# Kernel optimization log

Measured on AMD Instinct MI355X. Metric: run time of the kernel, lower is better.

## Reference

```python
import jax, jax.numpy as jnp
import numpy as np

N_HEADS = 16
KV_HEADS = 4
D_HEAD = 64
D_MODEL = 1024
NUM_BUCKETS = 32
MAX_DISTANCE = 128


def _relative_position_bucket(relative_position, num_buckets=NUM_BUCKETS, max_distance=MAX_DISTANCE):
    # Bidirectional (encoder) T5 bucket function.
    nb = num_buckets // 2
    rel_buckets = (relative_position > 0).astype(jnp.int32) * nb
    rp = jnp.abs(relative_position)
    max_exact = nb // 2
    is_small = rp < max_exact
    rp_safe = jnp.maximum(rp, 1).astype(jnp.float32)
    rp_large = max_exact + (
        jnp.log(rp_safe / max_exact) / np.log(max_distance / max_exact) * (nb - max_exact)
    ).astype(jnp.int32)
    rp_large = jnp.minimum(rp_large, nb - 1)
    return rel_buckets + jnp.where(is_small, rp, rp_large)


def compute_bias(rel_bias, q_len, k_len):
    context_pos = jnp.arange(q_len)[:, None]
    memory_pos = jnp.arange(k_len)[None, :]
    buckets = _relative_position_bucket(memory_pos - context_pos)  # [q, k]
    values = rel_bias[buckets]                                     # [q, k, H]
    return jnp.transpose(values, (2, 0, 1))[None]                  # [1, H, q, k]


def setup_inputs() -> dict:
    key = jax.random.key(0)
    ks = jax.random.split(key, 6)
    scale = D_MODEL ** -0.5
    return {
        "hidden_states": jax.random.normal(ks[0], (4, 2048, D_MODEL), jnp.float32),
        "Wq": jax.random.normal(ks[1], (N_HEADS * D_HEAD, D_MODEL), jnp.float32) * scale,
        "Wk": jax.random.normal(ks[2], (N_HEADS * D_HEAD, D_MODEL), jnp.float32) * scale,
        "Wv": jax.random.normal(ks[3], (N_HEADS * D_HEAD, D_MODEL), jnp.float32) * scale,
        "Wo": jax.random.normal(ks[4], (D_MODEL, N_HEADS * D_HEAD), jnp.float32) * scale,
        "rel_bias": jax.random.normal(ks[5], (NUM_BUCKETS, N_HEADS), jnp.float32),
    }


def reference(hidden_states, Wq, Wk, Wv, Wo, rel_bias):
    B, N, _ = hidden_states.shape
    G = N_HEADS // KV_HEADS
    # projections: torch Linear -> x @ W.T; shape to [b, heads, n, d]
    q = (hidden_states @ Wq.T).reshape(B, N, N_HEADS, D_HEAD).transpose(0, 2, 1, 3)
    k = (hidden_states @ Wk.T).reshape(B, N, N_HEADS, D_HEAD).transpose(0, 2, 1, 3)
    v = (hidden_states @ Wv.T).reshape(B, N, N_HEADS, D_HEAD).transpose(0, 2, 1, 3)
    # split heads into (g, h) groups with h = kv_heads as inner index
    gq = q.reshape(B, G, KV_HEADS, N, D_HEAD)
    gk = k.reshape(B, G, KV_HEADS, N, D_HEAD).mean(axis=1)  # [b, h, n, d]
    gv = v.reshape(B, G, KV_HEADS, N, D_HEAD).mean(axis=1)
    # NOTE: einsum sums queries over the group axis g (faithful to source)
    scores = jnp.einsum('bghnd,bhsd->bhns', gq, gk)
    bias = compute_bias(rel_bias, N, N)                      # [1, H, n, n]
    gbias = bias.reshape(1, G, KV_HEADS, N, N).mean(axis=1)  # [1, h, n, n]
    scores = scores + gbias
    attn = jax.nn.softmax(scores.astype(jnp.float32), axis=-1).astype(scores.dtype)
    out = jnp.einsum('bhns,bhsd->bhnd', attn, gv)
    out = out.transpose(0, 2, 1, 3).reshape(B, N, KV_HEADS * D_HEAD)
    out = jnp.tile(out, (1, 1, G))  # repeat 'b s d -> b s (g d)'
    return out @ Wo.T
```

## Files before the change

kernel.cpp:

```cpp
#include <hip/hip_runtime.h>
#include <math.h>

typedef _Float16 half_t;
typedef _Float16 half4 __attribute__((ext_vector_type(4)));
typedef _Float16 half8 __attribute__((ext_vector_type(8)));
typedef float f32x4 __attribute__((ext_vector_type(4)));

#define LOG2E 1.44269504088896f

__device__ __forceinline__ void gload16(const void* g, void* l) {
    __builtin_amdgcn_global_load_lds(
        (const __attribute__((address_space(1))) unsigned int*)g,
        (__attribute__((address_space(3))) unsigned int*)l, 16, 0, 0);
}

__global__ __launch_bounds__(256) void prep(const float* __restrict__ hs,
                     const float* __restrict__ Wq, const float* __restrict__ Wk,
                     const float* __restrict__ Wv, const float* __restrict__ Wo,
                     const float* __restrict__ rb,
                     half_t* __restrict__ hsh,
                     half_t* __restrict__ Wqkv, half_t* __restrict__ Wo_e,
                     float* __restrict__ btab) {
    if (blockIdx.x < 4096) {
        int i = (blockIdx.x * 256 + threadIdx.x) * 8;
        f32x4 a = *(const f32x4*)&hs[i];
        f32x4 b = *(const f32x4*)&hs[i + 4];
        half8 o;
        #pragma unroll
        for (int j = 0; j < 4; ++j) { o[j] = (half_t)a[j]; o[4 + j] = (half_t)b[j]; }
        *(half8*)&hsh[i] = o;
        return;
    }
    int idx = (blockIdx.x - 4096) * 256 + threadIdx.x;
    if (idx < 768 * 1024) {
        int row = idx >> 10, col = idx & 1023;
        int sec = row >> 8;
        int r = row & 255;
        int h = r >> 6, d = r & 63;
        const float* W = (sec == 0) ? Wq : ((sec == 1) ? Wk : Wv);
        float s = 0.f;
        #pragma unroll
        for (int g = 0; g < 4; ++g) s += W[((g * 4 + h) * 64 + d) * 1024 + col];
        s *= (sec == 0) ? LOG2E : 0.25f;
        Wqkv[idx] = (half_t)s;
    }
    if (idx < 1024 * 256) {
        int m = idx >> 8, c = idx & 255;
        float s = 0.f;
        #pragma unroll
        for (int g = 0; g < 4; ++g) s += Wo[m * 1024 + g * 256 + c];
        Wo_e[idx] = (half_t)s;
    }
    if (idx < 4 * 4096) {
        int h = idx >> 12, dpos = idx & 4095;
        int delta = dpos - 2048;
        int bucket = (delta > 0) ? 16 : 0;
        int ad = delta < 0 ? -delta : delta;
        if (ad < 8) bucket += ad;
        else {
            int large = 8 + (int)(logf((float)ad * 0.125f) / logf(16.0f) * 8.0f);
            bucket += (large < 15) ? large : 15;
        }
        float s = 0.f;
        #pragma unroll
        for (int g = 0; g < 4; ++g) s += rb[bucket * 16 + g * 4 + h];
        btab[idx] = s * 0.25f * LOG2E;
    }
}

__global__ __launch_bounds__(256) void gemm_nt_mfma(const half_t* __restrict__ A,
                                                    const half_t* __restrict__ B,
                                                    void* __restrict__ Cptr,
                                                    int M, int N, int K, int store_half,
                                                    half_t* __restrict__ vtp) {
    __shared__ __attribute__((aligned(16))) half_t As[128 * 64];
    __shared__ __attribute__((aligned(16))) half_t Bs[64 * 64];
    int tid = threadIdx.x;
    int w = tid >> 6, lane = tid & 63;
    int c = lane & 15, quad = lane >> 4;
    int rowBase = blockIdx.y * 128, colBase = blockIdx.x * 64;
    int wr = (w & 1) * 64, wc = (w >> 1) * 32;

    f32x4 acc[4][2];
    #pragma unroll
    for (int i = 0; i < 4; ++i)
        #pragma unroll
        for (int j = 0; j < 2; ++j) acc[i][j] = (f32x4)(0.f);

    int srow = tid >> 3;
    int kcs = ((tid & 7) ^ (srow & 7)) * 8;
    int rx = c & 7;

    for (int k0 = 0; k0 < K; k0 += 64) {
        __syncthreads();
        #pragma unroll
        for (int p = 0; p < 4; ++p)
            gload16(&A[(size_t)(rowBase + srow + 32 * p) * K + k0 + kcs],
                    &As[p * 2048 + w * 512]);
        #pragma unroll
        for (int p = 0; p < 2; ++p)
            gload16(&B[(size_t)(colBase + srow + 32 * p) * K + k0 + kcs],
                    &Bs[p * 2048 + w * 512]);
        __syncthreads();

        #pragma unroll
        for (int kh = 0; kh < 2; ++kh) {
            int xk = ((quad + 4 * kh) ^ rx) * 8;
            half8 af[4], bf[2];
            #pragma unroll
            for (int i = 0; i < 4; ++i)
                af[i] = *(const half8*)&As[(wr + i * 16 + c) * 64 + xk];
            #pragma unroll
            for (int j = 0; j < 2; ++j)
                bf[j] = *(const half8*)&Bs[(wc + j * 16 + c) * 64 + xk];
            #pragma unroll
            for (int i = 0; i < 4; ++i)
                #pragma unroll
                for (int j = 0; j < 2; ++j)
                    acc[i][j] = __builtin_amdgcn_mfma_f32_16x16x32_f16(af[i], bf[j], acc[i][j], 0, 0, 0);
        }
    }

    if (vtp && colBase >= 512) {
        int h = (colBase - 512) >> 6;
        #pragma unroll
        for (int i = 0; i < 4; ++i)
            #pragma unroll
            for (int j = 0; j < 2; ++j) {
                int row0 = rowBase + wr + i * 16 + quad * 4;
                int dd = wc + j * 16 + c;
                int b = row0 >> 11, n = row0 & 2047;
                half4 pk;
                #pragma unroll
                for (int reg = 0; reg < 4; ++reg) pk[reg] = (half_t)acc[i][j][reg];
                *(half4*)&vtp[((size_t)((b * 4 + h) * 64 + dd)) * 2048 + n] = pk;
            }
        return;
    }

    #pragma unroll
    for (int i = 0; i < 4; ++i)
        #pragma unroll
        for (int j = 0; j < 2; ++j)
            #pragma unroll
            for (int reg = 0; reg < 4; ++reg) {
                size_t row = rowBase + wr + i * 16 + quad * 4 + reg;
                size_t col = colBase + wc + j * 16 + c;
                if (store_half) ((half_t*)Cptr)[row * N + col] = (half_t)acc[i][j][reg];
                else            ((float*)Cptr)[row * N + col] = acc[i][j][reg];
            }
}

__global__ __launch_bounds__(256) void attn(const half_t* __restrict__ qkv,
                                            const half_t* __restrict__ vt,
                                            const float* __restrict__ btab,
                                            half_t* __restrict__ Opart,
                                            float* __restrict__ ml) {
    __shared__ __attribute__((aligned(16))) half_t Ks[64 * 64];
    __shared__ __attribute__((aligned(16))) half_t Vts[64 * 64];
    __shared__ __attribute__((aligned(16))) half_t Ps[4 * 16 * 72];
    __shared__ float bstat[1152];

    int tid = threadIdx.x;
    int w = tid >> 6, lane = tid & 63;
    int c = lane & 15, quad = lane >> 4;
    int qt = blockIdx.x, h = blockIdx.y;
    int b = blockIdx.z >> 1, s = blockIdx.z & 1;
    int q0 = qt * 64;
    int bh = b * 4 + h;
    int k0g = s * 1024;

    const half_t* qrow = qkv + (size_t)(b * 2048 + q0 + w * 16 + c) * 768 + h * 64;
    half8 qf0 = *(const half8*)(qrow + quad * 8);
    half8 qf1 = *(const half8*)(qrow + 32 + quad * 8);

    float cpos = btab[h * 4096 + 4095];
    float cneg = btab[h * 4096];

    int bbase = k0g - q0 - 63 + 2048;
    for (int j = tid; j < 1152; j += 256) {
        int gi = bbase + j;
        gi = gi < 0 ? 0 : (gi > 4095 ? 4095 : gi);
        bstat[j] = btab[h * 4096 + gi];
    }

    int srow = tid >> 3;
    int kcs = ((tid & 7) ^ (srow & 7)) * 8;
    const half_t* gK = qkv + (size_t)(b * 2048 + k0g + srow) * 768 + 256 + h * 64 + kcs;
    const half_t* gV = vt + (size_t)(bh * 64 + srow) * 2048 + k0g + kcs;

    f32x4 O[4];
    #pragma unroll
    for (int i = 0; i < 4; ++i) O[i] = (f32x4)(0.f);
    float mrow = -1e30f, lrow = 0.f;

    int rx = c & 7;
    half_t* pw = &Ps[w * 16 * 72];

    for (int it = 0; it < 16; ++it) {
        int ktg = k0g + it * 64;
        __syncthreads();
        {
            const half_t* gKt = gK + (size_t)(it * 64) * 768;
            const half_t* gVt = gV + it * 64;
            gload16(gKt,                     &Ks[w * 512]);
            gload16(gKt + (size_t)32 * 768,  &Ks[2048 + w * 512]);
            gload16(gVt,                     &Vts[w * 512]);
            gload16(gVt + 32 * 2048,         &Vts[2048 + w * 512]);
        }
        __syncthreads();

        f32x4 ST[4];
        #pragma unroll
        for (int kb = 0; kb < 4; ++kb) {
            int row = kb * 16 + c;
            half8 kf0 = *(const half8*)&Ks[row * 64 + (quad ^ rx) * 8];
            half8 kf1 = *(const half8*)&Ks[row * 64 + ((quad + 4) ^ rx) * 8];
            f32x4 a = (f32x4)(0.f);
            a = __builtin_amdgcn_mfma_f32_16x16x32_f16(kf0, qf0, a, 0, 0, 0);
            a = __builtin_amdgcn_mfma_f32_16x16x32_f16(kf1, qf1, a, 0, 0, 0);
            ST[kb] = a;
        }

        float cb;
        if (ktg >= q0 + 191) {
            cb = cpos;
        } else if (ktg + 191 <= q0) {
            cb = cneg;
        } else {
            cb = 0.f;
            int jb = it * 64 + 63 - (w * 16 + c);
            #pragma unroll
            for (int kb = 0; kb < 4; ++kb)
                #pragma unroll
                for (int rg = 0; rg < 4; ++rg)
                    ST[kb][rg] += bstat[jb + kb * 16 + quad * 4 + rg];
        }

        float tmax = -1e30f;
        #pragma unroll
        for (int kb = 0; kb < 4; ++kb)
            #pragma unroll
            for (int rg = 0; rg < 4; ++rg) tmax = fmaxf(tmax, ST[kb][rg]);
        tmax += cb;
        tmax = fmaxf(tmax, __shfl_xor(tmax, 16));
        tmax = fmaxf(tmax, __shfl_xor(tmax, 32));

        float mnew = fmaxf(mrow, tmax);
        float alpha = exp2f(mrow - mnew);
        mrow = mnew;
        float madj = mnew - cb;

        float lsum = 0.f;
        #pragma unroll
        for (int kb = 0; kb < 4; ++kb) {
            half4 pk;
            #pragma unroll
            for (int rg = 0; rg < 4; ++rg) {
                float p = exp2f(ST[kb][rg] - madj);
                lsum += p;
                pk[rg] = (half_t)p;
            }
            *(half4*)&pw[c * 72 + kb * 16 + quad * 4] = pk;
        }
        lrow = lrow * alpha + lsum;
        __asm__ __volatile__("s_waitcnt lgkmcnt(0)" ::: "memory");

        half8 pf0 = *(const half8*)&pw[c * 72 + quad * 8];
        half8 pf1 = *(const half8*)&pw[c * 72 + 32 + quad * 8];
        #pragma unroll
        for (int db = 0; db < 4; ++db) {
            int row = db * 16 + c;
            half8 vf0 = *(const half8*)&Vts[row * 64 + (quad ^ rx) * 8];
            half8 vf1 = *(const half8*)&Vts[row * 64 + ((quad + 4) ^ rx) * 8];
            f32x4 o = O[db];
            #pragma unroll
            for (int rg = 0; rg < 4; ++rg) o[rg] *= alpha;
            o = __builtin_amdgcn_mfma_f32_16x16x32_f16(vf0, pf0, o, 0, 0, 0);
            o = __builtin_amdgcn_mfma_f32_16x16x32_f16(vf1, pf1, o, 0, 0, 0);
            O[db] = o;
        }
    }

    lrow += __shfl_xor(lrow, 16);
    lrow += __shfl_xor(lrow, 32);
    float inv = 1.0f / lrow;

    int pb = (bh * 32 + qt) * 2 + s;
    #pragma unroll
    for (int db = 0; db < 4; ++db) {
        half4 pk;
        #pragma unroll
        for (int rg = 0; rg < 4; ++rg) pk[rg] = (half_t)(O[db][rg] * inv);
        *(half4*)&Opart[((size_t)pb * 64 + w * 16 + c) * 64 + db * 16 + quad * 4] = pk;
    }
    if (quad == 0) {
        ml[pb * 128 + w * 16 + c] = mrow;
        ml[pb * 128 + 64 + w * 16 + c] = lrow;
    }
}

__global__ __launch_bounds__(256) void merge(const half_t* __restrict__ Opart,
                                             const float* __restrict__ ml,
                                             half_t* __restrict__ ab) {
    int bq = blockIdx.x;
    int bh = bq >> 5, qt = bq & 31;
    int b = bh >> 2, h = bh & 3;
    int row = threadIdx.x >> 2;
    int cg = (threadIdx.x & 3) * 16;
    int p0 = bq * 2, p1 = p0 + 1;
    float m1 = ml[p0 * 128 + row], l1 = ml[p0 * 128 + 64 + row];
    float m2 = ml[p1 * 128 + row], l2 = ml[p1 * 128 + 64 + row];
    float m = fmaxf(m1, m2);
    float a1 = exp2f(m1 - m) * l1, a2 = exp2f(m2 - m) * l2;
    float inv = 1.f / (a1 + a2);
    float w1 = a1 * inv, w2 = a2 * inv;
    const half8* o1 = (const half8*)&Opart[((size_t)p0 * 64 + row) * 64 + cg];
    const half8* o2 = (const half8*)&Opart[((size_t)p1 * 64 + row) * 64 + cg];
    half_t* dst = ab + (size_t)(b * 2048 + qt * 64 + row) * 256 + h * 64 + cg;
    #pragma unroll
    for (int v = 0; v < 2; ++v) {
        half8 x = o1[v], y = o2[v], o;
        #pragma unroll
        for (int j = 0; j < 8; ++j)
            o[j] = (half_t)((float)x[j] * w1 + (float)y[j] * w2);
        *(half8*)(dst + v * 8) = o;
    }
}

extern "C" void kernel_launch(void* const* d_in, const int* in_sizes, int n_in,
                              void* d_out, int out_size, void* d_ws, size_t ws_size,
                              hipStream_t stream) {
    (void)in_sizes; (void)n_in; (void)out_size; (void)ws_size;
    const float* hs = (const float*)d_in[0];
    const float* Wq = (const float*)d_in[1];
    const float* Wk = (const float*)d_in[2];
    const float* Wv = (const float*)d_in[3];
    const float* Wo = (const float*)d_in[4];
    const float* rb = (const float*)d_in[5];

    char* p = (char*)d_ws;
    half_t* Wqkv = (half_t*)p;            p += 768 * 1024 * 2;
    half_t* Wo_e = (half_t*)p;            p += 1024 * 256 * 2;
    float*  btab = (float*)p;             p += 4 * 4096 * 4;
    char*   hshp = p;                     p += (size_t)8192 * 1024 * 2;
    half_t* qkv  = (half_t*)p;            p += (size_t)8192 * 768 * 2;
    half_t* vt   = (half_t*)p;            p += (size_t)16 * 64 * 2048 * 2;
    half_t* hsh   = (half_t*)hshp;
    half_t* Opart = (half_t*)hshp;
    float*  mlbuf = (float*)(hshp + (size_t)1024 * 64 * 64 * 2);
    half_t* ab    = (half_t*)(hshp + (size_t)9 * 1024 * 1024);
    float*  out  = (float*)d_out;

    prep<<<7168, 256, 0, stream>>>(hs, Wq, Wk, Wv, Wo, rb, hsh, Wqkv, Wo_e, btab);

    gemm_nt_mfma<<<dim3(12, 64), 256, 0, stream>>>(hsh, Wqkv, qkv, 8192, 768, 1024, 1, vt);

    attn<<<dim3(32, 4, 8), 256, 0, stream>>>(qkv, vt, btab, Opart, mlbuf);
    merge<<<512, 256, 0, stream>>>(Opart, mlbuf, ab);

    gemm_nt_mfma<<<dim3(16, 64), 256, 0, stream>>>(ab, Wo_e, out, 8192, 1024, 256, 0, nullptr);
}
```

Baseline: 178.7 us.

## Double-buffer K/V tiles in attention and raise wave priority around MFMAs

The attention kernel's K and V shared-memory tiles become ping-pong buffers. The next tile's global-to-LDS loads are issued before computing on the current tile, and each iteration ends with a single vmcnt wait plus barrier instead of two barriers. This is meant to hide global load latency behind the QK and PV MFMA work. s_setprio is also raised around the MFMA blocks. The cost is doubled K/V LDS usage, which may reduce how many blocks fit per CU.

```diff
diff --git a/kernel.cpp b/kernel.cpp
--- a/kernel.cpp
+++ b/kernel.cpp
@@ -156,8 +156,8 @@
                                             const float* __restrict__ btab,
                                             half_t* __restrict__ Opart,
                                             float* __restrict__ ml) {
-    __shared__ __attribute__((aligned(16))) half_t Ks[64 * 64];
-    __shared__ __attribute__((aligned(16))) half_t Vts[64 * 64];
+    __shared__ __attribute__((aligned(16))) half_t Ks[2][64 * 64];
+    __shared__ __attribute__((aligned(16))) half_t Vts[2][64 * 64];
     __shared__ __attribute__((aligned(16))) half_t Ps[4 * 16 * 72];
     __shared__ float bstat[1152];
 
@@ -189,6 +189,16 @@
     const half_t* gK = qkv + (size_t)(b * 2048 + k0g + srow) * 768 + 256 + h * 64 + kcs;
     const half_t* gV = vt + (size_t)(bh * 64 + srow) * 2048 + k0g + kcs;
 
+    auto stage = [&](int it2) {
+        int bb = it2 & 1;
+        const half_t* gKt = gK + (size_t)(it2 * 64) * 768;
+        const half_t* gVt = gV + it2 * 64;
+        gload16(gKt,                     &Ks[bb][w * 512]);
+        gload16(gKt + (size_t)32 * 768,  &Ks[bb][2048 + w * 512]);
+        gload16(gVt,                     &Vts[bb][w * 512]);
+        gload16(gVt + 32 * 2048,         &Vts[bb][2048 + w * 512]);
+    };
+
     f32x4 O[4];
     #pragma unroll
     for (int i = 0; i < 4; ++i) O[i] = (f32x4)(0.f);
@@ -197,30 +207,28 @@
     int rx = c & 7;
     half_t* pw = &Ps[w * 16 * 72];
 
+    stage(0);
+    __syncthreads();
+
     for (int it = 0; it < 16; ++it) {
         int ktg = k0g + it * 64;
-        __syncthreads();
-        {
-            const half_t* gKt = gK + (size_t)(it * 64) * 768;
-            const half_t* gVt = gV + it * 64;
-            gload16(gKt,                     &Ks[w * 512]);
-            gload16(gKt + (size_t)32 * 768,  &Ks[2048 + w * 512]);
-            gload16(gVt,                     &Vts[w * 512]);
-            gload16(gVt + 32 * 2048,         &Vts[2048 + w * 512]);
-        }
-        __syncthreads();
+        if (it < 15) stage(it + 1);
+        const half_t* Kb = Ks[it & 1];
+        const half_t* Vb = Vts[it & 1];
 
         f32x4 ST[4];
+        __builtin_amdgcn_s_setprio(1);
         #pragma unroll
         for (int kb = 0; kb < 4; ++kb) {
             int row = kb * 16 + c;
-            half8 kf0 = *(const half8*)&Ks[row * 64 + (quad ^ rx) * 8];
-            half8 kf1 = *(const half8*)&Ks[row * 64 + ((quad + 4) ^ rx) * 8];
+            half8 kf0 = *(const half8*)&Kb[row * 64 + (quad ^ rx) * 8];
+            half8 kf1 = *(const half8*)&Kb[row * 64 + ((quad + 4) ^ rx) * 8];
             f32x4 a = (f32x4)(0.f);
             a = __builtin_amdgcn_mfma_f32_16x16x32_f16(kf0, qf0, a, 0, 0, 0);
             a = __builtin_amdgcn_mfma_f32_16x16x32_f16(kf1, qf1, a, 0, 0, 0);
             ST[kb] = a;
         }
+        __builtin_amdgcn_s_setprio(0);
 
         float cb;
         if (ktg >= q0 + 191) {
@@ -268,11 +276,12 @@
 
         half8 pf0 = *(const half8*)&pw[c * 72 + quad * 8];
         half8 pf1 = *(const half8*)&pw[c * 72 + 32 + quad * 8];
+        __builtin_amdgcn_s_setprio(1);
         #pragma unroll
         for (int db = 0; db < 4; ++db) {
             int row = db * 16 + c;
-            half8 vf0 = *(const half8*)&Vts[row * 64 + (quad ^ rx) * 8];
-            half8 vf1 = *(const half8*)&Vts[row * 64 + ((quad + 4) ^ rx) * 8];
+            half8 vf0 = *(const half8*)&Vb[row * 64 + (quad ^ rx) * 8];
+            half8 vf1 = *(const half8*)&Vb[row * 64 + ((quad + 4) ^ rx) * 8];
             f32x4 o = O[db];
             #pragma unroll
             for (int rg = 0; rg < 4; ++rg) o[rg] *= alpha;
@@ -280,6 +289,10 @@
             o = __builtin_amdgcn_mfma_f32_16x16x32_f16(vf1, pf1, o, 0, 0, 0);
             O[db] = o;
         }
+        __builtin_amdgcn_s_setprio(0);
+
+        __asm__ __volatile__("s_waitcnt vmcnt(0)" ::: "memory");
+        __builtin_amdgcn_s_barrier();
     }
 
     lrow += __shfl_xor(lrow, 16);
```

Result: slower. 193.7 us (+8.4%).
